# Optimization experiments

Hardware: AMD Instinct MI355X
Metric: run time of the kernel (lower is better)

The kernel has to match this reference:

```python
import jax, jax.numpy as jnp
import numpy as np

BATCH = 2
SEQ = 2048
DIM = 2048
HEADS = 16
DIM_HEAD = 64
DIM_INNER = HEADS * DIM_HEAD  # 1024
SOFTCAP = 50.0
EPS = 1e-12


def setup_inputs() -> dict:
    key = jax.random.key(0)
    k1, k2, k3, k4 = jax.random.split(key, 4)
    x = jax.random.normal(k1, (BATCH, SEQ, DIM), dtype=jnp.float32)
    # RMSNorm gamma param (initialized near zero in the torch module)
    gamma = jax.random.normal(k2, (DIM,), dtype=jnp.float32) * 0.02
    # Linear weights stored already-transposed: x @ W
    w_qkv = jax.random.normal(k3, (DIM, 3 * DIM_INNER), dtype=jnp.float32) * (DIM ** -0.5)
    w_out = jax.random.normal(k4, (DIM_INNER, DIM), dtype=jnp.float32) * (DIM_INNER ** -0.5)
    # (type, offset, length) triples per batch; bidirectional attention inside each span
    modalities = jnp.array(
        [[[0, 256, 256], [0, 1024, 512]],
         [[0, 128, 256], [0, 1536, 384]]], dtype=jnp.int32)
    return dict(x=x, gamma=gamma, w_qkv=w_qkv, w_out=w_out, modalities=modalities)


def _transfusion_attn_mask(seq_len, modalities):
    # causal | (q in span AND kv in span)  -> Bool[b, i, j]
    seq = jnp.arange(seq_len)
    causal = seq[:, None] >= seq[None, :]                      # [i, j]
    offsets = modalities[..., 1]                                # [b, m]
    ends = offsets + modalities[..., 2]                         # [b, m]
    q_in = seq[None, None, :] >= offsets[..., None]             # [b, m, i]
    kv_in = seq[None, None, :] < ends[..., None]                # [b, m, j]
    is_modality = jnp.any(q_in[..., :, None] & kv_in[..., None, :], axis=1)  # [b, i, j]
    return causal[None] | is_modality


def _rmsnorm(x, gamma):
    n = jnp.sqrt(jnp.sum(x * x, axis=-1, keepdims=True))
    x = x / jnp.maximum(n, EPS)
    return x * (DIM ** 0.5) * (gamma + 1.0)


def reference(x, gamma, w_qkv, w_out, modalities):
    xn = _rmsnorm(x, gamma)
    qkv = xn @ w_qkv                                            # [b, n, 3*h*d]
    qkv = qkv.reshape(BATCH, SEQ, 3, HEADS, DIM_HEAD)
    qkv = jnp.transpose(qkv, (2, 0, 3, 1, 4))                   # [3, b, h, n, d]
    q, k, v = qkv[0], qkv[1], qkv[2]
    q = q * (DIM_HEAD ** -0.5)
    sim = jnp.einsum('bhid,bhjd->bhij', q, k)
    sim = jnp.tanh(sim / SOFTCAP) * SOFTCAP                     # softclamp
    mask = _transfusion_attn_mask(SEQ, modalities)              # [b, i, j]
    neg = -jnp.finfo(sim.dtype).max
    sim = jnp.where(mask[:, None, :, :], sim, neg)
    attn = jax.nn.softmax(sim, axis=-1)
    out = jnp.einsum('bhij,bhjd->bhid', attn, v)
    out = jnp.transpose(out, (0, 2, 1, 3)).reshape(BATCH, SEQ, DIM_INNER)
    return out @ w_out
```

## Files before the change

kernel.cpp:

```cpp
#include <hip/hip_runtime.h>
#include <hip/hip_bf16.h>

typedef unsigned short u16;
typedef unsigned int u32;
typedef __attribute__((ext_vector_type(8))) short short8;
typedef __attribute__((ext_vector_type(4))) float f32x4;
typedef __attribute__((ext_vector_type(4))) u16 u16x4;

#define DEV __device__ __forceinline__

DEV u16 f2bf(float f) {
    union { float f; u32 u; } v; v.f = f;
    u32 r = v.u;
    u32 lsb = (r >> 16) & 1u;
    r += 0x7fffu + lsb;
    return (u16)(r >> 16);
}

DEV void gload_lds16(const u16* g, u16* l) {
    __builtin_amdgcn_global_load_lds(
        (const __attribute__((address_space(1))) u32*)(const void*)g,
        (__attribute__((address_space(3))) u32*)(void*)l,
        16, 0, 0);
}

__global__ void prep(const float* __restrict__ x, const float* __restrict__ gamma,
                     const float* __restrict__ w_qkv, const float* __restrict__ w_out,
                     u16* __restrict__ xn, u16* __restrict__ wqkvT, u16* __restrict__ woutT) {
    __shared__ float tile[32][33];
    __shared__ float red[4];
    int id = blockIdx.x;
    int t = threadIdx.x;
    if (id < 8192) {
        const float* in; u16* out; int R, C, bx, by;
        if (id < 6144) { in = w_qkv; out = wqkvT; R = 2048; C = 3072; bx = id % 96; by = id / 96; }
        else { id -= 6144; in = w_out; out = woutT; R = 1024; C = 2048; bx = id % 64; by = id / 64; }
        int tx = t & 31, ty = t >> 5;
        int c0 = bx * 32, r0 = by * 32;
#pragma unroll
        for (int i = 0; i < 4; i++)
            tile[ty * 4 + i][tx] = in[(size_t)(r0 + ty * 4 + i) * C + c0 + tx];
        __syncthreads();
#pragma unroll
        for (int i = 0; i < 4; i++)
            out[(size_t)(c0 + ty * 4 + i) * R + r0 + tx] = f2bf(tile[tx][ty * 4 + i]);
    } else {
        int row = id - 8192;
        const float4* xr = (const float4*)(x + (size_t)row * 2048);
        float4 a = xr[t];
        float4 b = xr[256 + t];
        float ss = a.x * a.x + a.y * a.y + a.z * a.z + a.w * a.w +
                   b.x * b.x + b.y * b.y + b.z * b.z + b.w * b.w;
#pragma unroll
        for (int off = 32; off; off >>= 1) ss += __shfl_xor(ss, off);
        if ((t & 63) == 0) red[t >> 6] = ss;
        __syncthreads();
        float tot = red[0] + red[1] + red[2] + red[3];
        float n = sqrtf(tot);
        float inv = 45.254833995939045f / fmaxf(n, 1e-12f);
        const float4* gr = (const float4*)gamma;
        float4 g0 = gr[t], g1 = gr[256 + t];
        u16x4 o0 = { f2bf(a.x * inv * (g0.x + 1.f)), f2bf(a.y * inv * (g0.y + 1.f)),
                     f2bf(a.z * inv * (g0.z + 1.f)), f2bf(a.w * inv * (g0.w + 1.f)) };
        u16x4 o1 = { f2bf(b.x * inv * (g1.x + 1.f)), f2bf(b.y * inv * (g1.y + 1.f)),
                     f2bf(b.z * inv * (g1.z + 1.f)), f2bf(b.w * inv * (g1.w + 1.f)) };
        u16x4* xo = (u16x4*)(xn + (size_t)row * 2048);
        xo[t] = o0;
        xo[256 + t] = o1;
    }
}

template <int EPI, int BN, int CCOL>
__global__ __launch_bounds__(512, 1) void gemmcf(
    const u16* __restrict__ A, const u16* __restrict__ BT,
    int M, int N, int K,
    float* __restrict__ Cout,
    u16* __restrict__ qb, u16* __restrict__ kb, u16* __restrict__ vT) {
    constexpr int HN = BN / 2;
    constexpr int NF2 = BN / 64;
    constexpr int NG0 = (NF2 + 1) / 2;
    constexpr bool B2 = (HN * 8) > 512;
    __shared__ __align__(16) u16 As[2][2][8192];
    __shared__ __align__(16) u16 Bs[2][2][HN * 64];
    int t = threadIdx.x, lane = t & 63, wid = t >> 6;
    int g = lane >> 4, r = lane & 15;
    int wm = wid >> 2, wn = wid & 3;
    int bhalf = wn >> 1;
    int cb0w = (wn & 1) * (BN / 4);
    int rsw = r & 7;

    int id = blockIdx.x;
    int xcd = id & 7, slot = id >> 3;
    int by = (xcd >> 1) * 4 + slot / CCOL;
    int bx = (xcd & 1) * CCOL + slot % CCOL;
    int brow = by * 256, bcol = bx * BN;

    int gsl = (t & 7) ^ ((t >> 3) & 7);
    const u16* Ag = A + (size_t)(brow + (t >> 3)) * K + gsl * 8;
    const u16* Bg = BT + (size_t)(bcol + (t >> 3)) * K + gsl * 8;
    int dstc = t * 8;

    f32x4 acc[2][4][NF2] = {};
    short8 areg[4][2], breg[NF2][2];
    int NT = K >> 6;

#define STG_A(bf_, kt_, h_) { \
        gload_lds16(Ag + (size_t)((h_) * 128) * K + (kt_) * 64, &As[bf_][h_][dstc]); \
        gload_lds16(Ag + (size_t)((h_) * 128 + 64) * K + (kt_) * 64, &As[bf_][h_][4096 + dstc]); }
#define STG_B(bf_, kt_, h_) { \
        gload_lds16(Bg + (size_t)((h_) * HN) * K + (kt_) * 64, &Bs[bf_][h_][dstc]); \
        if constexpr (B2) { if (t < 256) \
            gload_lds16(Bg + (size_t)((h_) * HN + 64) * K + (kt_) * 64, &Bs[bf_][h_][4096 + dstc]); } }
#define RD_A(qm_) { \
    _Pragma("unroll") for (int mf = 0; mf < 4; mf++) \
    _Pragma("unroll") for (int ks = 0; ks < 2; ks++) \
        areg[mf][ks] = *(const short8*)&As[buf][qm_][(wm * 64 + mf * 16 + r) * 64 + (((ks << 2) + g) ^ rsw) * 8]; }
#define RD_B() { \
    _Pragma("unroll") for (int nf = 0; nf < NF2; nf++) \
    _Pragma("unroll") for (int ks = 0; ks < 2; ks++) \
        breg[nf][ks] = *(const short8*)&Bs[buf][bhalf][(cb0w + nf * 16 + r) * 64 + (((ks << 2) + g) ^ rsw) * 8]; }
#define MFMA_G(qm_, nf0_, nf1_) { \
    __builtin_amdgcn_s_setprio(1); \
    _Pragma("unroll") for (int ks = 0; ks < 2; ks++) \
    _Pragma("unroll") for (int mf = 0; mf < 4; mf++) \
    _Pragma("unroll") for (int nf = nf0_; nf < nf1_; nf++) \
        acc[qm_][mf][nf] = __builtin_amdgcn_mfma_f32_16x16x32_bf16( \
            areg[mf][ks], breg[nf][ks], acc[qm_][mf][nf], 0, 0, 0); \
    __builtin_amdgcn_s_setprio(0); }
#define SCHEDB() __builtin_amdgcn_sched_barrier(0)
#define BAR() __builtin_amdgcn_s_barrier()

    STG_A(0, 0, 0); STG_A(0, 0, 1); STG_B(0, 0, 0); STG_B(0, 0, 1);
    if (NT > 1) { STG_A(1, 1, 0); STG_A(1, 1, 1); }
    if (NT > 1) { asm volatile("s_waitcnt vmcnt(4)" ::: "memory"); }
    else        { asm volatile("s_waitcnt vmcnt(0)" ::: "memory"); }
    SCHEDB();
    BAR();

    for (int kt = 0; kt < NT; ++kt) {
        int buf = kt & 1, ob = buf ^ 1;
        bool s1 = kt + 1 < NT, s2 = kt + 2 < NT;

        RD_B(); RD_A(0);
        if (s1) STG_B(ob, kt + 1, 1);
        asm volatile("s_waitcnt lgkmcnt(0)" ::: "memory");
        SCHEDB();
        MFMA_G(0, 0, NG0);
        BAR();

        if (s1) STG_B(ob, kt + 1, 0);
        if (s2) STG_A(buf, kt + 2, 0);
        MFMA_G(0, NG0, NF2);
        BAR();

        RD_A(1);
        asm volatile("s_waitcnt lgkmcnt(0)" ::: "memory");
        SCHEDB();
        MFMA_G(1, 0, NG0);
        BAR();

        if (s2) STG_A(buf, kt + 2, 1);
        MFMA_G(1, NG0, NF2);
        if (s2)      { asm volatile("s_waitcnt vmcnt(4)" ::: "memory"); }
        else if (s1) { asm volatile("s_waitcnt vmcnt(0)" ::: "memory"); }
        SCHEDB();
        BAR();
    }
#undef STG_A
#undef STG_B
#undef RD_A
#undef RD_B
#undef MFMA_G
#undef SCHEDB
#undef BAR

    if (EPI == 0) {
#pragma unroll
        for (int qm = 0; qm < 2; qm++)
#pragma unroll
            for (int mf = 0; mf < 4; mf++)
#pragma unroll
                for (int nf = 0; nf < NF2; nf++) {
                    int cb = bcol + bhalf * HN + cb0w + nf * 16 + r;
                    int which = cb >> 10;
                    int hd = cb & 1023;
                    int hh = hd >> 6, d = hd & 63;
#pragma unroll
                    for (int j = 0; j < 4; j++) {
                        int rr = brow + qm * 128 + wm * 64 + mf * 16 + 4 * g + j;
                        int b = rr >> 11, nn = rr & 2047;
                        float v = acc[qm][mf][nf][j];
                        size_t bh = (size_t)(b * 16 + hh);
                        if (which == 0)      qb[(bh * 2048 + nn) * 64 + d] = f2bf(v * 0.125f);
                        else if (which == 1) kb[(bh * 2048 + nn) * 64 + d] = f2bf(v);
                        else                 vT[(bh * 64 + d) * 2048 + nn] = f2bf(v);
                    }
                }
    } else {
#pragma unroll
        for (int qm = 0; qm < 2; qm++)
#pragma unroll
            for (int mf = 0; mf < 4; mf++)
#pragma unroll
                for (int nf = 0; nf < NF2; nf++) {
                    int cb = bcol + bhalf * HN + cb0w + nf * 16 + r;
#pragma unroll
                    for (int j = 0; j < 4; j++) {
                        int rr = brow + qm * 128 + wm * 64 + mf * 16 + 4 * g + j;
                        Cout[(size_t)rr * N + cb] = acc[qm][mf][nf][j];
                    }
                }
    }
}

__global__ __launch_bounds__(256, 3) void flash_attn(
    const u16* __restrict__ q, const u16* __restrict__ kk, const u16* __restrict__ vT,
    const int* __restrict__ mods, u16* __restrict__ attn_out) {
    __shared__ __align__(16) u16 Ks[2][4096];
    __shared__ __align__(16) u16 Vs[2][4096];
    __shared__ __align__(16) u16 Plds[4][16][72];
    int t = threadIdx.x, lane = t & 63, wave = t >> 6;
    int g = lane >> 4, r = lane & 15;
    int h = blockIdx.x, b = blockIdx.y;
    int qs = (31 - blockIdx.z) * 64;
    int bh = b * 16 + h;
    int qbase = qs + wave * 16;

    int off0 = mods[b * 6 + 1], end0 = off0 + mods[b * 6 + 2];
    int off1 = mods[b * 6 + 4], end1 = off1 + mods[b * 6 + 5];

    const u16* Qp = q + ((size_t)bh * 2048 + qbase) * 64;
    short8 qf0 = *(const short8*)(Qp + (size_t)r * 64 + 8 * g);
    short8 qf1 = *(const short8*)(Qp + (size_t)r * 64 + 32 + 8 * g);

    int iq = qbase + r;
    int lim0 = (iq >= off0) ? end0 : 0;
    int lim1 = (iq >= off1) ? end1 : 0;
    int rowlim = max(iq + 1, max(lim0, lim1));

    int jlb = qs + 64;
    if (qs + 63 >= off0) jlb = max(jlb, end0);
    if (qs + 63 >= off1) jlb = max(jlb, end1);

    const u16* Kp = kk + (size_t)bh * 2048 * 64;
    const u16* Vp = vT + (size_t)bh * 64 * 2048;
    u16* Pw = &Plds[wave][0][0];

    f32x4 ot[4] = {};
    float psA = 0.f, psB = 0.f;
    int sw = r & 7;

    auto stage64 = [&](const u16* gbase, int gstride, u16* lds) {
#pragma unroll
        for (int i = 0; i < 2; i++) {
            int c = i * 256 + t;
            int row = c >> 3;
            int gsl = (c & 7) ^ (row & 7);
            gload_lds16(gbase + (size_t)row * gstride + 8 * gsl,
                        lds + (size_t)(c & ~63) * 8);
        }
    };

    stage64(Kp, 64, Ks[0]);
    stage64(Vp, 2048, Vs[0]);
    int buf = 0;

    for (int jb = 0; jb < jlb; jb += 64) {
        if (jb + 64 < jlb) {
            stage64(Kp + (size_t)(jb + 64) * 64, 64, Ks[buf ^ 1]);
            stage64(Vp + (jb + 64), 2048, Vs[buf ^ 1]);
            asm volatile("s_waitcnt vmcnt(4)" ::: "memory");
        } else {
            asm volatile("s_waitcnt vmcnt(0)" ::: "memory");
        }
        __builtin_amdgcn_s_barrier();
        const u16* Kt = Ks[buf];
        const u16* Vt = Vs[buf];

        f32x4 st[4];
#pragma unroll
        for (int tt = 0; tt < 4; tt++) {
            int row = 16 * tt + r;
            short8 kf0 = *(const short8*)&Kt[(size_t)(row * 8 + (g ^ sw)) * 8];
            short8 kf1 = *(const short8*)&Kt[(size_t)(row * 8 + ((4 + g) ^ sw)) * 8];
            f32x4 z = {};
            z = __builtin_amdgcn_mfma_f32_16x16x32_bf16(kf0, qf0, z, 0, 0, 0);
            z = __builtin_amdgcn_mfma_f32_16x16x32_bf16(kf1, qf1, z, 0, 0, 0);
            st[tt] = z;
        }
#pragma unroll
        for (int tt = 0; tt < 4; tt++) {
            int kvb = jb + 16 * tt + 4 * g;
            float p0, p1, p2, p3;
#pragma unroll
            for (int j = 0; j < 4; j++) {
                float x = st[tt][j];
                float x2 = x * x;
                float inner = __builtin_fmaf(x2, 2.1333333e-8f, -1.3333333e-4f);
                float poly = __builtin_fmaf(x2, inner, 1.0f);
                float pv = __expf(x * poly);
                pv = (kvb + j < rowlim) ? pv : 0.f;
                if (j == 0) p0 = pv; else if (j == 1) p1 = pv;
                else if (j == 2) p2 = pv; else p3 = pv;
            }
            psA += p0 + p1;
            psB += p2 + p3;
            u32 pk0, pk1;
            asm("v_cvt_pk_bf16_f32 %0, %1, %2" : "=v"(pk0) : "v"(p0), "v"(p1));
            asm("v_cvt_pk_bf16_f32 %0, %1, %2" : "=v"(pk1) : "v"(p2), "v"(p3));
            *(u32*)&Pw[r * 72 + 16 * tt + 4 * g] = pk0;
            *(u32*)&Pw[r * 72 + 16 * tt + 4 * g + 2] = pk1;
        }
        short8 pf0 = *(const short8*)&Pw[r * 72 + 8 * g];
        short8 pf1 = *(const short8*)&Pw[r * 72 + 32 + 8 * g];
#pragma unroll
        for (int dt = 0; dt < 4; dt++) {
            int row = 16 * dt + r;
            short8 vf0 = *(const short8*)&Vt[(size_t)(row * 8 + (g ^ sw)) * 8];
            short8 vf1 = *(const short8*)&Vt[(size_t)(row * 8 + ((4 + g) ^ sw)) * 8];
            ot[dt] = __builtin_amdgcn_mfma_f32_16x16x32_bf16(vf0, pf0, ot[dt], 0, 0, 0);
            ot[dt] = __builtin_amdgcn_mfma_f32_16x16x32_bf16(vf1, pf1, ot[dt], 0, 0, 0);
        }
        asm volatile("s_waitcnt lgkmcnt(0)" ::: "memory");
        __builtin_amdgcn_s_barrier();
        buf ^= 1;
    }

    float lrow = psA + psB;
    lrow += __shfl_xor(lrow, 16);
    lrow += __shfl_xor(lrow, 32);
    float inv = 1.f / lrow;
    u16* Op = attn_out + ((size_t)(b * 2048 + qbase + r)) * 1024 + h * 64;
#pragma unroll
    for (int dt = 0; dt < 4; dt++) {
        u16x4 o = { f2bf(ot[dt][0] * inv), f2bf(ot[dt][1] * inv),
                    f2bf(ot[dt][2] * inv), f2bf(ot[dt][3] * inv) };
        *(u16x4*)(Op + dt * 16 + 4 * g) = o;
    }
}

extern "C" void kernel_launch(void* const* d_in, const int* in_sizes, int n_in,
                              void* d_out, int out_size, void* d_ws, size_t ws_size,
                              hipStream_t stream) {
    const float* x = (const float*)d_in[0];
    const float* gamma = (const float*)d_in[1];
    const float* w_qkv = (const float*)d_in[2];
    const float* w_out = (const float*)d_in[3];
    const int* mods = (const int*)d_in[4];
    float* out = (float*)d_out;

    u16* ws = (u16*)d_ws;
    u16* xn    = ws;
    u16* wqkvT = ws + 8388608;
    u16* woutT = ws + 14680064;
    u16* qb    = ws + 16777216;
    u16* kb    = ws + 20971520;
    u16* vT    = ws + 25165824;
    u16* ao    = ws + 29360128;

    prep<<<dim3(12288), dim3(256), 0, stream>>>(x, gamma, w_qkv, w_out, xn, wqkvT, woutT);
    gemmcf<0, 192, 8><<<dim3(256), dim3(512), 0, stream>>>(xn, wqkvT, 4096, 3072, 2048,
                                                           nullptr, qb, kb, vT);
    flash_attn<<<dim3(16, 2, 32), dim3(256), 0, stream>>>(qb, kb, vT, mods, ao);
    gemmcf<1, 128, 8><<<dim3(256), dim3(512), 0, stream>>>(ao, woutT, 4096, 2048, 1024,
                                                           out, nullptr, nullptr, nullptr);
}
```

Baseline: 164.1 us.

## Replace GEMM with smaller-tile triple-buffered kernel; process two query tiles per attention wave

The GEMM kernel is rewritten. It now uses 128-row tiles, a K-step of 32 and three LDS buffers, and launches 512 blocks with launch bounds asking for multiple blocks per CU. This replaces the earlier 256-row, two-phase double-buffered schedule, with the aim of better occupancy and simpler latency hiding. Flash attention now gives each wave 32 query rows (two 16-row sub-tiles), so each K/V LDS fragment is reused for twice the MFMA work and the grid is halved. In exchange, per-tile reuse in the GEMM drops, registers grow in attention, and fewer attention blocks may leave causal load imbalance.

After: 179.3 us. 9.3% more time.

```diff
diff --git a/kernel.cpp b/kernel.cpp
--- a/kernel.cpp
+++ b/kernel.cpp
@@ -70,146 +70,116 @@
     }
 }
 
-template <int EPI, int BN, int CCOL>
-__global__ __launch_bounds__(512, 1) void gemmcf(
+template <int EPI, int BN>
+__global__ __launch_bounds__(512, 4) void gemmw(
     const u16* __restrict__ A, const u16* __restrict__ BT,
     int M, int N, int K,
     float* __restrict__ Cout,
     u16* __restrict__ qb, u16* __restrict__ kb, u16* __restrict__ vT) {
-    constexpr int HN = BN / 2;
-    constexpr int NF2 = BN / 64;
-    constexpr int NG0 = (NF2 + 1) / 2;
-    constexpr bool B2 = (HN * 8) > 512;
-    __shared__ __align__(16) u16 As[2][2][8192];
-    __shared__ __align__(16) u16 Bs[2][2][HN * 64];
+    constexpr int NF = BN / 64;
+    constexpr bool BX = (BN * 4) > 512;
+    __shared__ __align__(16) u16 As[3][4096];
+    __shared__ __align__(16) u16 Bs[3][BN * 32];
     int t = threadIdx.x, lane = t & 63, wid = t >> 6;
     int g = lane >> 4, r = lane & 15;
     int wm = wid >> 2, wn = wid & 3;
-    int bhalf = wn >> 1;
-    int cb0w = (wn & 1) * (BN / 4);
-    int rsw = r & 7;
 
     int id = blockIdx.x;
     int xcd = id & 7, slot = id >> 3;
-    int by = (xcd >> 1) * 4 + slot / CCOL;
-    int bx = (xcd & 1) * CCOL + slot % CCOL;
-    int brow = by * 256, bcol = bx * BN;
-
-    int gsl = (t & 7) ^ ((t >> 3) & 7);
-    const u16* Ag = A + (size_t)(brow + (t >> 3)) * K + gsl * 8;
-    const u16* Bg = BT + (size_t)(bcol + (t >> 3)) * K + gsl * 8;
-    int dstc = t * 8;
-
-    f32x4 acc[2][4][NF2] = {};
-    short8 areg[4][2], breg[NF2][2];
-    int NT = K >> 6;
-
-#define STG_A(bf_, kt_, h_) { \
-        gload_lds16(Ag + (size_t)((h_) * 128) * K + (kt_) * 64, &As[bf_][h_][dstc]); \
-        gload_lds16(Ag + (size_t)((h_) * 128 + 64) * K + (kt_) * 64, &As[bf_][h_][4096 + dstc]); }
-#define STG_B(bf_, kt_, h_) { \
-        gload_lds16(Bg + (size_t)((h_) * HN) * K + (kt_) * 64, &Bs[bf_][h_][dstc]); \
-        if constexpr (B2) { if (t < 256) \
-            gload_lds16(Bg + (size_t)((h_) * HN + 64) * K + (kt_) * 64, &Bs[bf_][h_][4096 + dstc]); } }
-#define RD_A(qm_) { \
-    _Pragma("unroll") for (int mf = 0; mf < 4; mf++) \
-    _Pragma("unroll") for (int ks = 0; ks < 2; ks++) \
-        areg[mf][ks] = *(const short8*)&As[buf][qm_][(wm * 64 + mf * 16 + r) * 64 + (((ks << 2) + g) ^ rsw) * 8]; }
-#define RD_B() { \
-    _Pragma("unroll") for (int nf = 0; nf < NF2; nf++) \
-    _Pragma("unroll") for (int ks = 0; ks < 2; ks++) \
-        breg[nf][ks] = *(const short8*)&Bs[buf][bhalf][(cb0w + nf * 16 + r) * 64 + (((ks << 2) + g) ^ rsw) * 8]; }
-#define MFMA_G(qm_, nf0_, nf1_) { \
-    __builtin_amdgcn_s_setprio(1); \
-    _Pragma("unroll") for (int ks = 0; ks < 2; ks++) \
-    _Pragma("unroll") for (int mf = 0; mf < 4; mf++) \
-    _Pragma("unroll") for (int nf = nf0_; nf < nf1_; nf++) \
-        acc[qm_][mf][nf] = __builtin_amdgcn_mfma_f32_16x16x32_bf16( \
-            areg[mf][ks], breg[nf][ks], acc[qm_][mf][nf], 0, 0, 0); \
-    __builtin_amdgcn_s_setprio(0); }
+    int by = (xcd >> 1) * 8 + (slot >> 3);
+    int bx = (xcd & 1) * 8 + (slot & 7);
+    int brow = by * 128, bcol = bx * BN;
+
+    const u16* Ag = A + (size_t)(brow + (t >> 2)) * K + (t & 3) * 8;
+    const u16* Bg = BT + (size_t)(bcol + (t >> 2)) * K + (t & 3) * 8;
+    const u16* Bg2 = BT + (size_t)(bcol + 128 + (t >> 2)) * K + (t & 3) * 8;
+    int dst = (t & ~63) * 8;
+
+    f32x4 acc[4][NF] = {};
+    short8 areg[4], breg[NF];
+    int NT = K >> 5;
+
+#define STG(kt_, b3_) { \
+        gload_lds16(Ag + (kt_) * 32, &As[b3_][dst]); \
+        gload_lds16(Bg + (kt_) * 32, &Bs[b3_][dst]); \
+        if constexpr (BX) { if (t < 256) gload_lds16(Bg2 + (kt_) * 32, &Bs[b3_][4096 + dst]); } }
 #define SCHEDB() __builtin_amdgcn_sched_barrier(0)
 #define BAR() __builtin_amdgcn_s_barrier()
 
-    STG_A(0, 0, 0); STG_A(0, 0, 1); STG_B(0, 0, 0); STG_B(0, 0, 1);
-    if (NT > 1) { STG_A(1, 1, 0); STG_A(1, 1, 1); }
-    if (NT > 1) { asm volatile("s_waitcnt vmcnt(4)" ::: "memory"); }
-    else        { asm volatile("s_waitcnt vmcnt(0)" ::: "memory"); }
+    STG(0, 0);
+    if (NT > 1) STG(1, 1);
+    asm volatile("s_waitcnt vmcnt(0)" ::: "memory");
     SCHEDB();
     BAR();
 
+    int c0 = 0;
     for (int kt = 0; kt < NT; ++kt) {
-        int buf = kt & 1, ob = buf ^ 1;
+        int c2 = c0 + 2; if (c2 >= 3) c2 -= 3;
         bool s1 = kt + 1 < NT, s2 = kt + 2 < NT;
-
-        RD_B(); RD_A(0);
-        if (s1) STG_B(ob, kt + 1, 1);
+        if (s2) STG(kt + 2, c2);
+        const u16* Ac = As[c0];
+        const u16* Bc = Bs[c0];
+#pragma unroll
+        for (int mf = 0; mf < 4; mf++)
+            areg[mf] = *(const short8*)&Ac[(wm * 64 + mf * 16 + r) * 32 + g * 8];
+#pragma unroll
+        for (int nf = 0; nf < NF; nf++)
+            breg[nf] = *(const short8*)&Bc[(wn * (BN / 4) + nf * 16 + r) * 32 + g * 8];
         asm volatile("s_waitcnt lgkmcnt(0)" ::: "memory");
         SCHEDB();
-        MFMA_G(0, 0, NG0);
-        BAR();
-
-        if (s1) STG_B(ob, kt + 1, 0);
-        if (s2) STG_A(buf, kt + 2, 0);
-        MFMA_G(0, NG0, NF2);
-        BAR();
-
-        RD_A(1);
-        asm volatile("s_waitcnt lgkmcnt(0)" ::: "memory");
-        SCHEDB();
-        MFMA_G(1, 0, NG0);
-        BAR();
-
-        if (s2) STG_A(buf, kt + 2, 1);
-        MFMA_G(1, NG0, NF2);
-        if (s2)      { asm volatile("s_waitcnt vmcnt(4)" ::: "memory"); }
-        else if (s1) { asm volatile("s_waitcnt vmcnt(0)" ::: "memory"); }
+        __builtin_amdgcn_s_setprio(1);
+#pragma unroll
+        for (int mf = 0; mf < 4; mf++)
+#pragma unroll
+            for (int nf = 0; nf < NF; nf++)
+                acc[mf][nf] = __builtin_amdgcn_mfma_f32_16x16x32_bf16(areg[mf], breg[nf], acc[mf][nf], 0, 0, 0);
+        __builtin_amdgcn_s_setprio(0);
+        if (s2) {
+            if (BX && wid < 4) { asm volatile("s_waitcnt vmcnt(3)" ::: "memory"); }
+            else               { asm volatile("s_waitcnt vmcnt(2)" ::: "memory"); }
+        } else if (s1) {
+            asm volatile("s_waitcnt vmcnt(0)" ::: "memory");
+        }
         SCHEDB();
         BAR();
-    }
-#undef STG_A
-#undef STG_B
-#undef RD_A
-#undef RD_B
-#undef MFMA_G
+        c0 = (c0 + 1 == 3) ? 0 : c0 + 1;
+    }
+#undef STG
 #undef SCHEDB
 #undef BAR
 
     if (EPI == 0) {
 #pragma unroll
-        for (int qm = 0; qm < 2; qm++)
-#pragma unroll
-            for (int mf = 0; mf < 4; mf++)
-#pragma unroll
-                for (int nf = 0; nf < NF2; nf++) {
-                    int cb = bcol + bhalf * HN + cb0w + nf * 16 + r;
-                    int which = cb >> 10;
-                    int hd = cb & 1023;
-                    int hh = hd >> 6, d = hd & 63;
-#pragma unroll
-                    for (int j = 0; j < 4; j++) {
-                        int rr = brow + qm * 128 + wm * 64 + mf * 16 + 4 * g + j;
-                        int b = rr >> 11, nn = rr & 2047;
-                        float v = acc[qm][mf][nf][j];
-                        size_t bh = (size_t)(b * 16 + hh);
-                        if (which == 0)      qb[(bh * 2048 + nn) * 64 + d] = f2bf(v * 0.125f);
-                        else if (which == 1) kb[(bh * 2048 + nn) * 64 + d] = f2bf(v);
-                        else                 vT[(bh * 64 + d) * 2048 + nn] = f2bf(v);
-                    }
+        for (int mf = 0; mf < 4; mf++)
+#pragma unroll
+            for (int nf = 0; nf < NF; nf++) {
+                int cb = bcol + wn * (BN / 4) + nf * 16 + r;
+                int which = cb >> 10;
+                int hd = cb & 1023;
+                int hh = hd >> 6, d = hd & 63;
+#pragma unroll
+                for (int j = 0; j < 4; j++) {
+                    int rr = brow + wm * 64 + mf * 16 + 4 * g + j;
+                    int b = rr >> 11, nn = rr & 2047;
+                    float v = acc[mf][nf][j];
+                    size_t bh = (size_t)(b * 16 + hh);
+                    if (which == 0)      qb[(bh * 2048 + nn) * 64 + d] = f2bf(v * 0.125f);
+                    else if (which == 1) kb[(bh * 2048 + nn) * 64 + d] = f2bf(v);
+                    else                 vT[(bh * 64 + d) * 2048 + nn] = f2bf(v);
                 }
+            }
     } else {
 #pragma unroll
-        for (int qm = 0; qm < 2; qm++)
-#pragma unroll
-            for (int mf = 0; mf < 4; mf++)
-#pragma unroll
-                for (int nf = 0; nf < NF2; nf++) {
-                    int cb = bcol + bhalf * HN + cb0w + nf * 16 + r;
-#pragma unroll
-                    for (int j = 0; j < 4; j++) {
-                        int rr = brow + qm * 128 + wm * 64 + mf * 16 + 4 * g + j;
-                        Cout[(size_t)rr * N + cb] = acc[qm][mf][nf][j];
-                    }
+        for (int mf = 0; mf < 4; mf++)
+#pragma unroll
+            for (int nf = 0; nf < NF; nf++) {
+                int cb = bcol + wn * (BN / 4) + nf * 16 + r;
+#pragma unroll
+                for (int j = 0; j < 4; j++) {
+                    int rr = brow + wm * 64 + mf * 16 + 4 * g + j;
+                    Cout[(size_t)rr * N + cb] = acc[mf][nf][j];
                 }
+            }
     }
 }
 
@@ -218,36 +188,43 @@
     const int* __restrict__ mods, u16* __restrict__ attn_out) {
     __shared__ __align__(16) u16 Ks[2][4096];
     __shared__ __align__(16) u16 Vs[2][4096];
-    __shared__ __align__(16) u16 Plds[4][16][72];
+    __shared__ __align__(16) u16 Plds[4][2][16][72];
     int t = threadIdx.x, lane = t & 63, wave = t >> 6;
     int g = lane >> 4, r = lane & 15;
     int h = blockIdx.x, b = blockIdx.y;
-    int qs = (31 - blockIdx.z) * 64;
+    int qs = (15 - blockIdx.z) * 128;
     int bh = b * 16 + h;
-    int qbase = qs + wave * 16;
+    int qbase = qs + wave * 32;
 
     int off0 = mods[b * 6 + 1], end0 = off0 + mods[b * 6 + 2];
     int off1 = mods[b * 6 + 4], end1 = off1 + mods[b * 6 + 5];
 
     const u16* Qp = q + ((size_t)bh * 2048 + qbase) * 64;
-    short8 qf0 = *(const short8*)(Qp + (size_t)r * 64 + 8 * g);
-    short8 qf1 = *(const short8*)(Qp + (size_t)r * 64 + 32 + 8 * g);
-
-    int iq = qbase + r;
-    int lim0 = (iq >= off0) ? end0 : 0;
-    int lim1 = (iq >= off1) ? end1 : 0;
-    int rowlim = max(iq + 1, max(lim0, lim1));
-
-    int jlb = qs + 64;
-    if (qs + 63 >= off0) jlb = max(jlb, end0);
-    if (qs + 63 >= off1) jlb = max(jlb, end1);
+    short8 qf0[2], qf1[2];
+#pragma unroll
+    for (int s = 0; s < 2; s++) {
+        qf0[s] = *(const short8*)(Qp + (size_t)(s * 16 + r) * 64 + 8 * g);
+        qf1[s] = *(const short8*)(Qp + (size_t)(s * 16 + r) * 64 + 32 + 8 * g);
+    }
+
+    int rowlim[2];
+#pragma unroll
+    for (int s = 0; s < 2; s++) {
+        int iq = qbase + s * 16 + r;
+        int lim0 = (iq >= off0) ? end0 : 0;
+        int lim1 = (iq >= off1) ? end1 : 0;
+        rowlim[s] = max(iq + 1, max(lim0, lim1));
+    }
+
+    int jlb = qs + 128;
+    if (qs + 127 >= off0) jlb = max(jlb, end0);
+    if (qs + 127 >= off1) jlb = max(jlb, end1);
 
     const u16* Kp = kk + (size_t)bh * 2048 * 64;
     const u16* Vp = vT + (size_t)bh * 64 * 2048;
-    u16* Pw = &Plds[wave][0][0];
-
-    f32x4 ot[4] = {};
-    float psA = 0.f, psB = 0.f;
+
+    f32x4 ot[2][4] = {};
+    float psA[2] = {}, psB[2] = {};
     int sw = r & 7;
 
     auto stage64 = [&](const u16* gbase, int gstride, u16* lds) {
@@ -277,65 +254,82 @@
         const u16* Kt = Ks[buf];
         const u16* Vt = Vs[buf];
 
-        f32x4 st[4];
+        f32x4 st[2][4];
 #pragma unroll
         for (int tt = 0; tt < 4; tt++) {
             int row = 16 * tt + r;
             short8 kf0 = *(const short8*)&Kt[(size_t)(row * 8 + (g ^ sw)) * 8];
             short8 kf1 = *(const short8*)&Kt[(size_t)(row * 8 + ((4 + g) ^ sw)) * 8];
-            f32x4 z = {};
-            z = __builtin_amdgcn_mfma_f32_16x16x32_bf16(kf0, qf0, z, 0, 0, 0);
-            z = __builtin_amdgcn_mfma_f32_16x16x32_bf16(kf1, qf1, z, 0, 0, 0);
-            st[tt] = z;
-        }
-#pragma unroll
-        for (int tt = 0; tt < 4; tt++) {
-            int kvb = jb + 16 * tt + 4 * g;
-            float p0, p1, p2, p3;
-#pragma unroll
-            for (int j = 0; j < 4; j++) {
-                float x = st[tt][j];
-                float x2 = x * x;
-                float inner = __builtin_fmaf(x2, 2.1333333e-8f, -1.3333333e-4f);
-                float poly = __builtin_fmaf(x2, inner, 1.0f);
-                float pv = __expf(x * poly);
-                pv = (kvb + j < rowlim) ? pv : 0.f;
-                if (j == 0) p0 = pv; else if (j == 1) p1 = pv;
-                else if (j == 2) p2 = pv; else p3 = pv;
-            }
-            psA += p0 + p1;
-            psB += p2 + p3;
-            u32 pk0, pk1;
-            asm("v_cvt_pk_bf16_f32 %0, %1, %2" : "=v"(pk0) : "v"(p0), "v"(p1));
-            asm("v_cvt_pk_bf16_f32 %0, %1, %2" : "=v"(pk1) : "v"(p2), "v"(p3));
-            *(u32*)&Pw[r * 72 + 16 * tt + 4 * g] = pk0;
-            *(u32*)&Pw[r * 72 + 16 * tt + 4 * g + 2] = pk1;
-        }
-        short8 pf0 = *(const short8*)&Pw[r * 72 + 8 * g];
-        short8 pf1 = *(const short8*)&Pw[r * 72 + 32 + 8 * g];
+#pragma unroll
+            for (int s = 0; s < 2; s++) {
+                f32x4 z = {};
+                z = __builtin_amdgcn_mfma_f32_16x16x32_bf16(kf0, qf0[s], z, 0, 0, 0);
+                z = __builtin_amdgcn_mfma_f32_16x16x32_bf16(kf1, qf1[s], z, 0, 0, 0);
+                st[s][tt] = z;
+            }
+        }
+#pragma unroll
+        for (int s = 0; s < 2; s++) {
+            u16* Pws = &Plds[wave][s][0][0];
+#pragma unroll
+            for (int tt = 0; tt < 4; tt++) {
+                int kvb = jb + 16 * tt + 4 * g;
+                float p0, p1, p2, p3;
+#pragma unroll
+                for (int j = 0; j < 4; j++) {
+                    float x = st[s][tt][j];
+                    float x2 = x * x;
+                    float inner = __builtin_fmaf(x2, 2.1333333e-8f, -1.3333333e-4f);
+                    float poly = __builtin_fmaf(x2, inner, 1.0f);
+                    float pv = __expf(x * poly);
+                    pv = (kvb + j < rowlim[s]) ? pv : 0.f;
+                    if (j == 0) p0 = pv; else if (j == 1) p1 = pv;
+                    else if (j == 2) p2 = pv; else p3 = pv;
+                }
+                psA[s] += p0 + p1;
+                psB[s] += p2 + p3;
+                u32 pk0, pk1;
+                asm("v_cvt_pk_bf16_f32 %0, %1, %2" : "=v"(pk0) : "v"(p0), "v"(p1));
+                asm("v_cvt_pk_bf16_f32 %0, %1, %2" : "=v"(pk1) : "v"(p2), "v"(p3));
+                *(u32*)&Pws[r * 72 + 16 * tt + 4 * g] = pk0;
+                *(u32*)&Pws[r * 72 + 16 * tt + 4 * g + 2] = pk1;
+            }
+        }
+        short8 pf0[2], pf1[2];
+#pragma unroll
+        for (int s = 0; s < 2; s++) {
+            pf0[s] = *(const short8*)&Plds[wave][s][r][8 * g];
+            pf1[s] = *(const short8*)&Plds[wave][s][r][32 + 8 * g];
+        }
 #pragma unroll
         for (int dt = 0; dt < 4; dt++) {
             int row = 16 * dt + r;
             short8 vf0 = *(const short8*)&Vt[(size_t)(row * 8 + (g ^ sw)) * 8];
             short8 vf1 = *(const short8*)&Vt[(size_t)(row * 8 + ((4 + g) ^ sw)) * 8];
-            ot[dt] = __builtin_amdgcn_mfma_f32_16x16x32_bf16(vf0, pf0, ot[dt], 0, 0, 0);
-            ot[dt] = __builtin_amdgcn_mfma_f32_16x16x32_bf16(vf1, pf1, ot[dt], 0, 0, 0);
+#pragma unroll
+            for (int s = 0; s < 2; s++) {
+                ot[s][dt] = __builtin_amdgcn_mfma_f32_16x16x32_bf16(vf0, pf0[s], ot[s][dt], 0, 0, 0);
+                ot[s][dt] = __builtin_amdgcn_mfma_f32_16x16x32_bf16(vf1, pf1[s], ot[s][dt], 0, 0, 0);
+            }
         }
         asm volatile("s_waitcnt lgkmcnt(0)" ::: "memory");
         __builtin_amdgcn_s_barrier();
         buf ^= 1;
     }
 
-    float lrow = psA + psB;
-    lrow += __shfl_xor(lrow, 16);
-    lrow += __shfl_xor(lrow, 32);
-    float inv = 1.f / lrow;
-    u16* Op = attn_out + ((size_t)(b * 2048 + qbase + r)) * 1024 + h * 64;
-#pragma unroll
-    for (int dt = 0; dt < 4; dt++) {
-        u16x4 o = { f2bf(ot[dt][0] * inv), f2bf(ot[dt][1] * inv),
-                    f2bf(ot[dt][2] * inv), f2bf(ot[dt][3] * inv) };
-        *(u16x4*)(Op + dt * 16 + 4 * g) = o;
+#pragma unroll
+    for (int s = 0; s < 2; s++) {
+        float lrow = psA[s] + psB[s];
+        lrow += __shfl_xor(lrow, 16);
+        lrow += __shfl_xor(lrow, 32);
+        float inv = 1.f / lrow;
+        u16* Op = attn_out + ((size_t)(b * 2048 + qbase + s * 16 + r)) * 1024 + h * 64;
+#pragma unroll
+        for (int dt = 0; dt < 4; dt++) {
+            u16x4 o = { f2bf(ot[s][dt][0] * inv), f2bf(ot[s][dt][1] * inv),
+                        f2bf(ot[s][dt][2] * inv), f2bf(ot[s][dt][3] * inv) };
+            *(u16x4*)(Op + dt * 16 + 4 * g) = o;
+        }
     }
 }
 
@@ -359,9 +353,9 @@
     u16* ao    = ws + 29360128;
 
     prep<<<dim3(12288), dim3(256), 0, stream>>>(x, gamma, w_qkv, w_out, xn, wqkvT, woutT);
-    gemmcf<0, 192, 8><<<dim3(256), dim3(512), 0, stream>>>(xn, wqkvT, 4096, 3072, 2048,
-                                                           nullptr, qb, kb, vT);
-    flash_attn<<<dim3(16, 2, 32), dim3(256), 0, stream>>>(qb, kb, vT, mods, ao);
-    gemmcf<1, 128, 8><<<dim3(256), dim3(512), 0, stream>>>(ao, woutT, 4096, 2048, 1024,
-                                                           out, nullptr, nullptr, nullptr);
-}
+    gemmw<0, 192><<<dim3(512), dim3(512), 0, stream>>>(xn, wqkvT, 4096, 3072, 2048,
+                                                       nullptr, qb, kb, vT);
+    flash_attn<<<dim3(16, 2, 16), dim3(256), 0, stream>>>(qb, kb, vT, mods, ao);
+    gemmw<1, 128><<<dim3(512), dim3(512), 0, stream>>>(ao, woutT, 4096, 2048, 1024,
+                                                       out, nullptr, nullptr, nullptr);
+}
```
